# Performance work log

Hardware: AMD Instinct MI355X
Metric: run time of the kernel (lower is better)

Reference implementation:

```python
import jax, jax.numpy as jnp
import numpy as np

N_NODES = 100000
N_EDGES = 1000000
D = 64
HID = 64
OUT = 64
N_CLS = 10
N_GRAPHS = 512
BN_EPS = 1e-5


def setup_inputs() -> dict:
    key = jax.random.key(0)
    ks = jax.random.split(key, 16)
    inp = {
        "x": jax.random.normal(ks[0], (N_NODES, D), dtype=jnp.float32),
        "edge_index": jax.random.randint(ks[1], (2, N_EDGES), 0, N_NODES, dtype=jnp.int32),
        "batch": jnp.sort(jax.random.randint(ks[2], (N_NODES,), 0, N_GRAPHS, dtype=jnp.int32)),
    }
    def lin(k, fi, fo):
        lim = 1.0 / np.sqrt(fi)
        kw, kb = jax.random.split(k)
        return (jax.random.uniform(kw, (fi, fo), minval=-lim, maxval=lim, dtype=jnp.float32),
                jax.random.uniform(kb, (fo,), minval=-lim, maxval=lim, dtype=jnp.float32))
    # conv0 MLP([64,64,64]) with BN after first linear
    inp["w0a"], inp["b0a"] = lin(ks[3], D, HID)
    inp["g0"] = jnp.ones((HID,), jnp.float32); inp["be0"] = jnp.zeros((HID,), jnp.float32)
    inp["m0"] = jnp.zeros((HID,), jnp.float32); inp["v0"] = jnp.ones((HID,), jnp.float32)
    inp["w0b"], inp["b0b"] = lin(ks[4], HID, HID)
    # conv1 MLP([64,64,64])
    inp["w1a"], inp["b1a"] = lin(ks[5], HID, HID)
    inp["g1"] = jnp.ones((HID,), jnp.float32); inp["be1"] = jnp.zeros((HID,), jnp.float32)
    inp["m1"] = jnp.zeros((HID,), jnp.float32); inp["v1"] = jnp.ones((HID,), jnp.float32)
    inp["w1b"], inp["b1b"] = lin(ks[6], HID, OUT)
    # classifier
    inp["wc"], inp["bc"] = lin(ks[7], OUT, N_CLS)
    return inp


def _bn_eval(h, g, b, m, v):
    return (h - m) * jax.lax.rsqrt(v + BN_EPS) * g + b


def _mlp(h, wa, ba, g, be, m, v, wb, bb):
    # Linear -> BN -> ReLU -> (dropout eval=identity) -> Linear
    h = h @ wa + ba
    h = jax.nn.relu(_bn_eval(h, g, be, m, v))
    return h @ wb + bb


def _gin_conv(h, src, dst, wa, ba, g, be, m, v, wb, bb):
    # GINConv eps=0: mlp(x + sum_{j->i} x_j), messages scatter-added at dst
    agg = jax.ops.segment_sum(h[src], dst, num_segments=N_NODES)
    return _mlp(h + agg, wa, ba, g, be, m, v, wb, bb)


def reference(x, edge_index, batch,
              w0a, b0a, g0, be0, m0, v0, w0b, b0b,
              w1a, b1a, g1, be1, m1, v1, w1b, b1b,
              wc, bc):
    src, dst = edge_index[0], edge_index[1]
    h = _gin_conv(x, src, dst, w0a, b0a, g0, be0, m0, v0, w0b, b0b)
    h = jax.nn.relu(h)  # dropout is identity in eval
    h = _gin_conv(h, src, dst, w1a, b1a, g1, be1, m1, v1, w1b, b1b)
    # global mean pool over batch indices
    sums = jax.ops.segment_sum(h, batch, num_segments=N_GRAPHS)
    cnts = jax.ops.segment_sum(jnp.ones((h.shape[0],), h.dtype), batch, num_segments=N_GRAPHS)
    pooled = sums / jnp.maximum(cnts, 1.0)[:, None]
    return pooled @ wc + bc
```

## Files before the change

kernel.cpp:

```cpp
#include <hip/hip_runtime.h>

#define N_NODES 100000
#define N_EDGES 1000000
#define N_GRAPHS 512
#define N_CLS 10
#define BN_EPS 1e-5f

#define SCAN_NB 200
#define NTILES2 3125

typedef _Float16 half8 __attribute__((ext_vector_type(8)));
typedef _Float16 half4v __attribute__((ext_vector_type(4)));
typedef float floatx4 __attribute__((ext_vector_type(4)));

__global__ __launch_bounds__(256) void prep_kernel(
    const float* __restrict__ x, _Float16* __restrict__ xh,
    const int* __restrict__ batch, const int* __restrict__ dstI,
    int* __restrict__ deg, int* __restrict__ rank,
    const float* __restrict__ w0a, const float* __restrict__ b0a,
    const float* __restrict__ g0, const float* __restrict__ be0,
    const float* __restrict__ m0, const float* __restrict__ v0,
    const float* __restrict__ w0b,
    const float* __restrict__ w1a, const float* __restrict__ b1a,
    const float* __restrict__ g1, const float* __restrict__ be1,
    const float* __restrict__ m1, const float* __restrict__ v1,
    const float* __restrict__ w1b,
    int* __restrict__ gstart,
    _Float16* __restrict__ wHi, _Float16* __restrict__ wLo,
    float* __restrict__ b1p0, float* __restrict__ b1p1) {
    const int gid = blockIdx.x * 256 + threadIdx.x;

    if (gid < 1600000) {
        float4 v = ((const float4*)x)[gid];
        half4v h = {(_Float16)v.x, (_Float16)v.y, (_Float16)v.z, (_Float16)v.w};
        ((half4v*)xh)[gid] = h;
    }

    if (gid < N_EDGES)
        rank[gid] = atomicAdd(&deg[dstI[gid]], 1);

    if (gid <= N_NODES) {
        int bcur = (gid < N_NODES) ? batch[gid] : N_GRAPHS;
        int bprev = (gid > 0) ? batch[gid - 1] : -1;
        for (int g = bprev + 1; g <= bcur; ++g) gstart[g] = gid;
    }

    if (gid < 16384) {
        const int e = gid & 4095, mat = gid >> 12;
        const int jj = e & 7, lane = (e >> 3) & 63, c = (e >> 9) & 3, k0 = (e >> 11) & 1;
        const int k = k0 * 32 + (lane >> 4) * 8 + jj;
        const int col = c * 16 + (lane & 15);
        float val;
        if (mat == 0)      val = w0a[k * 64 + col] * (rsqrtf(v0[col] + BN_EPS) * g0[col]);
        else if (mat == 1) val = w0b[k * 64 + col];
        else if (mat == 2) val = w1a[k * 64 + col] * (rsqrtf(v1[col] + BN_EPS) * g1[col]);
        else               val = w1b[k * 64 + col];
        _Float16 hi = (_Float16)val;
        wHi[gid] = hi;
        wLo[gid] = (_Float16)(val - (float)hi);
    }

    if (gid >= 16384 && gid < 16512) {
        int t = gid - 16384;
        if (t < 64) {
            float s = rsqrtf(v0[t] + BN_EPS) * g0[t];
            b1p0[t] = (b0a[t] - m0[t]) * s + be0[t];
        } else {
            t -= 64;
            float s = rsqrtf(v1[t] + BN_EPS) * g1[t];
            b1p1[t] = (b1a[t] - m1[t]) * s + be1[t];
        }
    }
}

__global__ __launch_bounds__(256) void scanA_kernel(const int* __restrict__ deg,
                                                    int* __restrict__ bsum) {
    __shared__ int sh[256];
    const int base = blockIdx.x * 512;
    const int t = threadIdx.x;
    int a = 0, b = 0;
    if (base + t < N_NODES) a = deg[base + t];
    if (base + 256 + t < N_NODES) b = deg[base + 256 + t];
    sh[t] = a + b;
    __syncthreads();
#pragma unroll
    for (int off = 128; off > 0; off >>= 1) {
        if (t < off) sh[t] += sh[t + off];
        __syncthreads();
    }
    if (t == 0) bsum[blockIdx.x] = sh[0];
}

__global__ __launch_bounds__(256) void scanC_kernel(const int* __restrict__ deg,
                                                    const int* __restrict__ bsum,
                                                    int* __restrict__ rowptr) {
    __shared__ int sh[256];
    __shared__ int sboff[256];
    const int base = blockIdx.x * 512;
    const int t = threadIdx.x;

    const int bv = (t < SCAN_NB) ? bsum[t] : 0;
    sboff[t] = bv;

    const int i0 = base + 2 * t, i1 = i0 + 1;
    const int d0 = (i0 < N_NODES) ? deg[i0] : 0;
    const int d1 = (i1 < N_NODES) ? deg[i1] : 0;
    const int p = d0 + d1;
    sh[t] = p;
    __syncthreads();
#pragma unroll
    for (int off = 1; off < 256; off <<= 1) {
        int u = (t >= off) ? sh[t - off] : 0;
        int ub = (t >= off) ? sboff[t - off] : 0;
        __syncthreads();
        sh[t] += u;
        sboff[t] += ub;
        __syncthreads();
    }
    const int myoff = (blockIdx.x == 0) ? 0 : sboff[blockIdx.x - 1];
    const int excl = myoff + sh[t] - p;
    if (i0 < N_NODES) rowptr[i0] = excl;
    if (i1 < N_NODES) rowptr[i1] = excl + d0;
    if (blockIdx.x == 0 && t == 0) rowptr[N_NODES] = N_EDGES;
}

__global__ __launch_bounds__(256) void fill_kernel(const int* __restrict__ srcI,
                                                   const int* __restrict__ dstI,
                                                   const int* __restrict__ rank,
                                                   const int* __restrict__ rowptr,
                                                   int* __restrict__ sortedSrc) {
    int e = blockIdx.x * 256 + threadIdx.x;
    if (e >= N_EDGES) return;
    sortedSrc[rowptr[dstI[e]] + rank[e]] = srcI[e];
}

__device__ __forceinline__ int swz(int row, int col) {
    return row * 64 + (col ^ ((row & 7) << 3));
}

__device__ __forceinline__ void idx_stage(const int* __restrict__ srcList, int rpv,
                                          int mq, int nodeSel, int slotSel, int& idxOwn) {
    const int rr0 = __shfl(rpv, mq * 4 + nodeSel, 64);
    const int rr1 = __shfl(rpv, mq * 4 + nodeSel + 1, 64);
    const int c = rr1 - rr0;
    const int e0 = (c > 0) ? min(slotSel, c - 1) : 0;
    int pos = rr0 + e0;
    pos = min(pos, N_EDGES - 1);
    idxOwn = srcList[pos];
}

__device__ __forceinline__ void rows_stage(const _Float16* __restrict__ in, int rpv,
                                           int mq, int strip0, int eoff, int lf,
                                           int idxOwn, half4v (&vT)[4][4], half4v (&sS)[4]) {
    const int m0 = mq * 4;
#pragma unroll
    for (int i = 0; i < 4; ++i) {
        sS[i] = (half4v){0, 0, 0, 0};
        if (eoff == 0)
            sS[i] = *(const half4v*)(in + (size_t)(strip0 + m0 + i) * 64 + lf * 4);
    }
#pragma unroll
    for (int i = 0; i < 4; ++i) {
        const int rr0 = __builtin_amdgcn_readlane(rpv, m0 + i);
        const int rr1 = __builtin_amdgcn_readlane(rpv, m0 + i + 1);
        const int cI = rr1 - rr0;
        const int g = (min(cI, 16) + 3) >> 2;
#pragma unroll
        for (int k = 0; k < 4; ++k) {
            vT[i][k] = (half4v){0, 0, 0, 0};
            if (k < g) {
                const int id = __shfl(idxOwn, i * 16 + 4 * k + eoff, 64);
                vT[i][k] = *(const half4v*)(in + (size_t)id * 64 + lf * 4);
            }
        }
    }
}

__device__ __forceinline__ void consume_stage(const _Float16* __restrict__ in,
                                              const int* __restrict__ srcList, int rpv,
                                              int mq, int eoff, int lf, int j,
                                              const half4v (&vT)[4][4], const half4v (&sS)[4],
                                              _Float16* aggH, _Float16* aggL) {
    const int m0 = mq * 4;
#pragma unroll
    for (int i = 0; i < 4; ++i) {
        const int rr0 = __builtin_amdgcn_readlane(rpv, m0 + i);
        const int rr1 = __builtin_amdgcn_readlane(rpv, m0 + i + 1);
        const int cI = rr1 - rr0;
        float aR[4] = {0.f, 0.f, 0.f, 0.f};
#pragma unroll
        for (int k = 0; k < 4; ++k) {
            if (4 * k + eoff < cI) {
                aR[0] += (float)vT[i][k].x; aR[1] += (float)vT[i][k].y;
                aR[2] += (float)vT[i][k].z; aR[3] += (float)vT[i][k].w;
            }
        }
        for (int eb = 16; eb < cI; eb += 16) {
#pragma unroll
            for (int k = 0; k < 4; ++k) {
                const int e_ = eb + 4 * k + eoff;
                if (e_ < cI) {
                    const int id = srcList[rr0 + e_];
                    half4v t = *(const half4v*)(in + (size_t)id * 64 + lf * 4);
                    aR[0] += (float)t.x; aR[1] += (float)t.y;
                    aR[2] += (float)t.z; aR[3] += (float)t.w;
                }
            }
        }
        if (eoff == 0) {
            aR[0] += (float)sS[i].x; aR[1] += (float)sS[i].y;
            aR[2] += (float)sS[i].z; aR[3] += (float)sS[i].w;
        }
#pragma unroll
        for (int q = 0; q < 4; ++q) {
            aR[q] += __shfl_xor(aR[q], 16, 64);
            aR[q] += __shfl_xor(aR[q], 32, 64);
        }
        if (j < 16) {
            half4v hi, lo;
#pragma unroll
            for (int q = 0; q < 4; ++q) {
                hi[q] = (_Float16)aR[q];
                lo[q] = (_Float16)(aR[q] - (float)hi[q]);
            }
            const int idx = swz(m0 + i, 4 * j);
            *(half4v*)(aggH + idx) = hi;
            *(half4v*)(aggL + idx) = lo;
        }
    }
}

#define SBAR() __builtin_amdgcn_sched_barrier(0)

template <int POOL>
__global__ __launch_bounds__(128, 4) void conv_mfma(
    const _Float16* __restrict__ in, const int* __restrict__ rowptr,
    const int* __restrict__ srcList,
    const _Float16* __restrict__ wH1, const _Float16* __restrict__ wL1,
    const _Float16* __restrict__ wH2, const _Float16* __restrict__ wL2,
    const float* __restrict__ b1, const float* __restrict__ b2,
    _Float16* __restrict__ out, const int* __restrict__ batch,
    float* __restrict__ pooled) {
    __shared__ __align__(16) unsigned char scratch[2][4096];

    const int tid = threadIdx.x;
    const int j = tid & 63, wv = tid >> 6;
    const int eoff = j >> 4;
    const int lf = j & 15;
    const int base = blockIdx.x * 32;
    const int strip0 = base + wv * 16;

    int bb = 0;
    if (POOL) bb = batch[strip0 + min(j, 15)];

    const int rpv = rowptr[strip0 + min(j, 16)];

    _Float16* aggH = (_Float16*)scratch[wv];
    _Float16* aggL = aggH + 1024;

    {
        int idxA, idxB, idxC;
        half4v vA[4][4], vB[4][4], sA[4], sB[4];

        idx_stage(srcList, rpv, 0, eoff, lf, idxA);
        idx_stage(srcList, rpv, 1, eoff, lf, idxB);
        SBAR();
        rows_stage(in, rpv, 0, strip0, eoff, lf, idxA, vA, sA);
        SBAR();
        idx_stage(srcList, rpv, 2, eoff, lf, idxC);
        SBAR();
        rows_stage(in, rpv, 1, strip0, eoff, lf, idxB, vB, sB);
        SBAR();
        consume_stage(in, srcList, rpv, 0, eoff, lf, j, vA, sA, aggH, aggL);
        SBAR();
        idx_stage(srcList, rpv, 3, eoff, lf, idxA);
        SBAR();
        rows_stage(in, rpv, 2, strip0, eoff, lf, idxC, vA, sA);
        SBAR();
        consume_stage(in, srcList, rpv, 1, eoff, lf, j, vB, sB, aggH, aggL);
        SBAR();
        rows_stage(in, rpv, 3, strip0, eoff, lf, idxA, vB, sB);
        SBAR();
        consume_stage(in, srcList, rpv, 2, eoff, lf, j, vA, sA, aggH, aggL);
        SBAR();
        consume_stage(in, srcList, rpv, 3, eoff, lf, j, vB, sB, aggH, aggL);
    }

    const int l15 = j & 15, quad = j >> 4;
    const floatx4 vzero = {0.f, 0.f, 0.f, 0.f};

    floatx4 acc[4] = {vzero, vzero, vzero, vzero};
    {
#pragma unroll
        for (int k0 = 0; k0 < 2; ++k0) {
            const int aidx = swz(l15, quad * 8 + k0 * 32);
            half8 aH = *(const half8*)(aggH + aidx);
            half8 aL = *(const half8*)(aggL + aidx);
#pragma unroll
            for (int c = 0; c < 4; ++c) {
                const int fo = ((k0 * 4 + c) * 64 + j) * 8;
                half8 bH = *(const half8*)(wH1 + fo);
                half8 bL = *(const half8*)(wL1 + fo);
                acc[c] = __builtin_amdgcn_mfma_f32_16x16x32_f16(aH, bH, acc[c], 0, 0, 0);
                acc[c] = __builtin_amdgcn_mfma_f32_16x16x32_f16(aL, bH, acc[c], 0, 0, 0);
                acc[c] = __builtin_amdgcn_mfma_f32_16x16x32_f16(aH, bL, acc[c], 0, 0, 0);
            }
        }
    }
    _Float16* hH = aggH;
    _Float16* hL = aggL;
#pragma unroll
    for (int c = 0; c < 4; ++c) {
        const float bv = b1[c * 16 + l15];
#pragma unroll
        for (int r = 0; r < 4; ++r) {
            const int idx = swz(quad * 4 + r, c * 16 + l15);
            float v = acc[c][r] + bv;
            v = fmaxf(v, 0.f);
            const _Float16 hi = (_Float16)v;
            hH[idx] = hi;
            hL[idx] = (_Float16)(v - (float)hi);
        }
    }

    floatx4 acc2[4] = {vzero, vzero, vzero, vzero};
    {
#pragma unroll
        for (int k0 = 0; k0 < 2; ++k0) {
            const int aidx = swz(l15, quad * 8 + k0 * 32);
            half8 aH = *(const half8*)(hH + aidx);
            half8 aL = *(const half8*)(hL + aidx);
#pragma unroll
            for (int c = 0; c < 4; ++c) {
                const int fo = ((k0 * 4 + c) * 64 + j) * 8;
                half8 bH = *(const half8*)(wH2 + fo);
                half8 bL = *(const half8*)(wL2 + fo);
                acc2[c] = __builtin_amdgcn_mfma_f32_16x16x32_f16(aH, bH, acc2[c], 0, 0, 0);
                acc2[c] = __builtin_amdgcn_mfma_f32_16x16x32_f16(aL, bH, acc2[c], 0, 0, 0);
                acc2[c] = __builtin_amdgcn_mfma_f32_16x16x32_f16(aH, bL, acc2[c], 0, 0, 0);
            }
        }
    }

    if (!POOL) {
#pragma unroll
        for (int c = 0; c < 4; ++c) {
            const float bv = b2[c * 16 + l15];
#pragma unroll
            for (int r = 0; r < 4; ++r) {
                const int node = strip0 + quad * 4 + r;
                out[(size_t)node * 64 + c * 16 + l15] =
                    (_Float16)fmaxf(acc2[c][r] + bv, 0.f);
            }
        }
    } else {
        float* oT = (float*)scratch[wv];
#pragma unroll
        for (int c = 0; c < 4; ++c) {
            const float bv = b2[c * 16 + l15];
#pragma unroll
            for (int r = 0; r < 4; ++r)
                oT[(quad * 4 + r) * 64 + c * 16 + l15] = acc2[c][r] + bv;
        }
        __builtin_amdgcn_s_waitcnt(0);
        int curB = -1;
        float accv = 0.f;
#pragma unroll
        for (int r = 0; r < 16; ++r) {
            const int b = __builtin_amdgcn_readlane(bb, r);
            const float v = oT[r * 64 + j];
            if (b != curB) {
                if (curB >= 0) atomicAdd(&pooled[curB * 64 + j], accv);
                curB = b;
                accv = v;
            } else {
                accv += v;
            }
        }
        atomicAdd(&pooled[curB * 64 + j], accv);
    }
}

__global__ __launch_bounds__(64) void classifier_kernel(const float* __restrict__ pooled,
                                                        const int* __restrict__ gstart,
                                                        const float* __restrict__ wc,
                                                        const float* __restrict__ bc,
                                                        float* __restrict__ out) {
    const int g = blockIdx.x;
    const int j = threadIdx.x;
    const float c = fmaxf((float)(gstart[g + 1] - gstart[g]), 1.f);
    const float mean = pooled[g * 64 + j] / c;
#pragma unroll
    for (int cc = 0; cc < N_CLS; ++cc) {
        float p = mean * wc[j * N_CLS + cc];
#pragma unroll
        for (int off = 32; off > 0; off >>= 1) p += __shfl_down(p, off, 64);
        if (j == 0) out[g * N_CLS + cc] = p + bc[cc];
    }
}


extern "C" void kernel_launch(void* const* d_in, const int* in_sizes, int n_in,
                              void* d_out, int out_size, void* d_ws, size_t ws_size,
                              hipStream_t stream) {
    const float* x   = (const float*)d_in[0];
    const int*   ei  = (const int*)d_in[1];
    const int* batch = (const int*)d_in[2];
    const float* w0a = (const float*)d_in[3];
    const float* b0a = (const float*)d_in[4];
    const float* g0  = (const float*)d_in[5];
    const float* be0 = (const float*)d_in[6];
    const float* m0  = (const float*)d_in[7];
    const float* v0  = (const float*)d_in[8];
    const float* w0b = (const float*)d_in[9];
    const float* b0b = (const float*)d_in[10];
    const float* w1a = (const float*)d_in[11];
    const float* b1a = (const float*)d_in[12];
    const float* g1  = (const float*)d_in[13];
    const float* be1 = (const float*)d_in[14];
    const float* m1  = (const float*)d_in[15];
    const float* v1  = (const float*)d_in[16];
    const float* w1b = (const float*)d_in[17];
    const float* b1b = (const float*)d_in[18];
    const float* wc  = (const float*)d_in[19];
    const float* bc  = (const float*)d_in[20];
    float* out = (float*)d_out;

    const int* srcI = ei;
    const int* dstI = ei + N_EDGES;

    int* ws = (int*)d_ws;
    int*      deg       = ws;
    int*      bsum      = ws + 100000;
    float*    pooled    = (float*)(ws + 100404);
    int*      rowptr    = ws + 133172;
    int*      rank      = ws + 233176;
    int*      sortedSrc = ws + 1233176;
    _Float16* xh        = (_Float16*)(ws + 2233176);
    _Float16* h1        = (_Float16*)(ws + 5433176);
    float*    b1p0      = (float*)(ws + 8633176);
    float*    b1p1      = (float*)(ws + 8633240);
    int*      gstart    = ws + 8633304;
    _Float16* wHi       = (_Float16*)(ws + 8633820);
    _Float16* wLo       = (_Float16*)(ws + 8642012);

    (void)hipMemsetAsync((void*)deg, 0, 133172 * sizeof(int), stream);
    prep_kernel<<<6250, 256, 0, stream>>>(x, xh, batch, dstI, deg, rank,
                                          w0a, b0a, g0, be0, m0, v0, w0b,
                                          w1a, b1a, g1, be1, m1, v1, w1b,
                                          gstart, wHi, wLo, b1p0, b1p1);

    scanA_kernel<<<SCAN_NB, 256, 0, stream>>>(deg, bsum);
    scanC_kernel<<<SCAN_NB, 256, 0, stream>>>(deg, bsum, rowptr);
    fill_kernel<<<(N_EDGES + 255) / 256, 256, 0, stream>>>(srcI, dstI, rank, rowptr, sortedSrc);

    conv_mfma<0><<<NTILES2, 128, 0, stream>>>(xh, rowptr, sortedSrc,
                                              wHi, wLo, wHi + 4096, wLo + 4096,
                                              b1p0, b0b, h1, nullptr, nullptr);

    conv_mfma<1><<<NTILES2, 128, 0, stream>>>(h1, rowptr, sortedSrc,
                                              wHi + 8192, wLo + 8192, wHi + 12288, wLo + 12288,
                                              b1p1, b1b, nullptr, batch, pooled);

    classifier_kernel<<<N_GRAPHS, 64, 0, stream>>>(pooled, gstart, wc, bc, out);
}
```

Baseline: 279.1 us.

## Merge memset, prep, scan and fill stages into one cooperative kernel

Replaces the memset, the prep kernel, the two scan kernels and the CSR fill kernel with a single cooperative launch of 1024 blocks. Grid-wide syncs separate the phases: zeroing and conversion, the degree atomics, the block sums, the prefix scan and the fill. Work is spread with grid-stride loops. The goal is to remove several launch and inter-kernel gaps, but each grid.sync has its own cost and the fixed grid size may reduce parallelism in the atomic and fill phases.

```diff
diff --git a/kernel.cpp b/kernel.cpp
--- a/kernel.cpp
+++ b/kernel.cpp
@@ -1,4 +1,7 @@
 #include <hip/hip_runtime.h>
+#include <hip/hip_cooperative_groups.h>
+
+namespace cg = cooperative_groups;
 
 #define N_NODES 100000
 #define N_EDGES 1000000
@@ -8,15 +11,20 @@
 
 #define SCAN_NB 200
 #define NTILES2 3125
+#define COOP_NB 1024
 
 typedef _Float16 half8 __attribute__((ext_vector_type(8)));
 typedef _Float16 half4v __attribute__((ext_vector_type(4)));
 typedef float floatx4 __attribute__((ext_vector_type(4)));
 
-__global__ __launch_bounds__(256) void prep_kernel(
+__global__ __launch_bounds__(256) void prologue_kernel(
     const float* __restrict__ x, _Float16* __restrict__ xh,
-    const int* __restrict__ batch, const int* __restrict__ dstI,
+    const int* __restrict__ batch,
+    const int* __restrict__ srcI, const int* __restrict__ dstI,
     int* __restrict__ deg, int* __restrict__ rank,
+    int* __restrict__ bsum, int* __restrict__ rowptr,
+    int* __restrict__ sortedSrc,
+    int* __restrict__ gstart,
     const float* __restrict__ w0a, const float* __restrict__ b0a,
     const float* __restrict__ g0, const float* __restrict__ be0,
     const float* __restrict__ m0, const float* __restrict__ v0,
@@ -25,28 +33,31 @@
     const float* __restrict__ g1, const float* __restrict__ be1,
     const float* __restrict__ m1, const float* __restrict__ v1,
     const float* __restrict__ w1b,
-    int* __restrict__ gstart,
     _Float16* __restrict__ wHi, _Float16* __restrict__ wLo,
     float* __restrict__ b1p0, float* __restrict__ b1p1) {
-    const int gid = blockIdx.x * 256 + threadIdx.x;
-
-    if (gid < 1600000) {
-        float4 v = ((const float4*)x)[gid];
+    __shared__ int sh[256];
+    __shared__ int sboff[256];
+
+    cg::grid_group grid = cg::this_grid();
+    const int tid0 = blockIdx.x * 256 + threadIdx.x;
+    const int NTH = COOP_NB * 256;
+
+    for (int i = tid0; i < 133172; i += NTH) deg[i] = 0;
+
+    for (int i = tid0; i < 1600000; i += NTH) {
+        float4 v = ((const float4*)x)[i];
         half4v h = {(_Float16)v.x, (_Float16)v.y, (_Float16)v.z, (_Float16)v.w};
-        ((half4v*)xh)[gid] = h;
-    }
-
-    if (gid < N_EDGES)
-        rank[gid] = atomicAdd(&deg[dstI[gid]], 1);
-
-    if (gid <= N_NODES) {
-        int bcur = (gid < N_NODES) ? batch[gid] : N_GRAPHS;
-        int bprev = (gid > 0) ? batch[gid - 1] : -1;
-        for (int g = bprev + 1; g <= bcur; ++g) gstart[g] = gid;
-    }
-
-    if (gid < 16384) {
-        const int e = gid & 4095, mat = gid >> 12;
+        ((half4v*)xh)[i] = h;
+    }
+
+    for (int i = tid0; i <= N_NODES; i += NTH) {
+        int bcur = (i < N_NODES) ? batch[i] : N_GRAPHS;
+        int bprev = (i > 0) ? batch[i - 1] : -1;
+        for (int g = bprev + 1; g <= bcur; ++g) gstart[g] = i;
+    }
+
+    if (tid0 < 16384) {
+        const int e = tid0 & 4095, mat = tid0 >> 12;
         const int jj = e & 7, lane = (e >> 3) & 63, c = (e >> 9) & 3, k0 = (e >> 11) & 1;
         const int k = k0 * 32 + (lane >> 4) * 8 + jj;
         const int col = c * 16 + (lane & 15);
@@ -56,12 +67,10 @@
         else if (mat == 2) val = w1a[k * 64 + col] * (rsqrtf(v1[col] + BN_EPS) * g1[col]);
         else               val = w1b[k * 64 + col];
         _Float16 hi = (_Float16)val;
-        wHi[gid] = hi;
-        wLo[gid] = (_Float16)(val - (float)hi);
-    }
-
-    if (gid >= 16384 && gid < 16512) {
-        int t = gid - 16384;
+        wHi[tid0] = hi;
+        wLo[tid0] = (_Float16)(val - (float)hi);
+    } else if (tid0 < 16512) {
+        int t = tid0 - 16384;
         if (t < 64) {
             float s = rsqrtf(v0[t] + BN_EPS) * g0[t];
             b1p0[t] = (b0a[t] - m0[t]) * s + be0[t];
@@ -71,67 +80,65 @@
             b1p1[t] = (b1a[t] - m1[t]) * s + be1[t];
         }
     }
-}
-
-__global__ __launch_bounds__(256) void scanA_kernel(const int* __restrict__ deg,
-                                                    int* __restrict__ bsum) {
-    __shared__ int sh[256];
-    const int base = blockIdx.x * 512;
-    const int t = threadIdx.x;
-    int a = 0, b = 0;
-    if (base + t < N_NODES) a = deg[base + t];
-    if (base + 256 + t < N_NODES) b = deg[base + 256 + t];
-    sh[t] = a + b;
-    __syncthreads();
-#pragma unroll
-    for (int off = 128; off > 0; off >>= 1) {
-        if (t < off) sh[t] += sh[t + off];
+
+    grid.sync();
+
+    for (int e = tid0; e < N_EDGES; e += NTH)
+        rank[e] = atomicAdd(&deg[dstI[e]], 1);
+
+    grid.sync();
+
+    if (blockIdx.x < SCAN_NB) {
+        const int base = blockIdx.x * 512;
+        const int t = threadIdx.x;
+        int a = 0, b = 0;
+        if (base + t < N_NODES) a = deg[base + t];
+        if (base + 256 + t < N_NODES) b = deg[base + 256 + t];
+        sh[t] = a + b;
         __syncthreads();
-    }
-    if (t == 0) bsum[blockIdx.x] = sh[0];
-}
-
-__global__ __launch_bounds__(256) void scanC_kernel(const int* __restrict__ deg,
-                                                    const int* __restrict__ bsum,
-                                                    int* __restrict__ rowptr) {
-    __shared__ int sh[256];
-    __shared__ int sboff[256];
-    const int base = blockIdx.x * 512;
-    const int t = threadIdx.x;
-
-    const int bv = (t < SCAN_NB) ? bsum[t] : 0;
-    sboff[t] = bv;
-
-    const int i0 = base + 2 * t, i1 = i0 + 1;
-    const int d0 = (i0 < N_NODES) ? deg[i0] : 0;
-    const int d1 = (i1 < N_NODES) ? deg[i1] : 0;
-    const int p = d0 + d1;
-    sh[t] = p;
-    __syncthreads();
-#pragma unroll
-    for (int off = 1; off < 256; off <<= 1) {
-        int u = (t >= off) ? sh[t - off] : 0;
-        int ub = (t >= off) ? sboff[t - off] : 0;
+#pragma unroll
+        for (int off = 128; off > 0; off >>= 1) {
+            if (t < off) sh[t] += sh[t + off];
+            __syncthreads();
+        }
+        if (t == 0) bsum[blockIdx.x] = sh[0];
+    }
+
+    grid.sync();
+
+    if (blockIdx.x < SCAN_NB) {
+        const int base = blockIdx.x * 512;
+        const int t = threadIdx.x;
+
+        const int bv = (t < SCAN_NB) ? bsum[t] : 0;
+        sboff[t] = bv;
+
+        const int i0 = base + 2 * t, i1 = i0 + 1;
+        const int d0 = (i0 < N_NODES) ? deg[i0] : 0;
+        const int d1 = (i1 < N_NODES) ? deg[i1] : 0;
+        const int p = d0 + d1;
+        sh[t] = p;
         __syncthreads();
-        sh[t] += u;
-        sboff[t] += ub;
-        __syncthreads();
-    }
-    const int myoff = (blockIdx.x == 0) ? 0 : sboff[blockIdx.x - 1];
-    const int excl = myoff + sh[t] - p;
-    if (i0 < N_NODES) rowptr[i0] = excl;
-    if (i1 < N_NODES) rowptr[i1] = excl + d0;
-    if (blockIdx.x == 0 && t == 0) rowptr[N_NODES] = N_EDGES;
-}
-
-__global__ __launch_bounds__(256) void fill_kernel(const int* __restrict__ srcI,
-                                                   const int* __restrict__ dstI,
-                                                   const int* __restrict__ rank,
-                                                   const int* __restrict__ rowptr,
-                                                   int* __restrict__ sortedSrc) {
-    int e = blockIdx.x * 256 + threadIdx.x;
-    if (e >= N_EDGES) return;
-    sortedSrc[rowptr[dstI[e]] + rank[e]] = srcI[e];
+#pragma unroll
+        for (int off = 1; off < 256; off <<= 1) {
+            int u = (t >= off) ? sh[t - off] : 0;
+            int ub = (t >= off) ? sboff[t - off] : 0;
+            __syncthreads();
+            sh[t] += u;
+            sboff[t] += ub;
+            __syncthreads();
+        }
+        const int myoff = (blockIdx.x == 0) ? 0 : sboff[blockIdx.x - 1];
+        const int excl = myoff + sh[t] - p;
+        if (i0 < N_NODES) rowptr[i0] = excl;
+        if (i1 < N_NODES) rowptr[i1] = excl + d0;
+        if (blockIdx.x == 0 && t == 0) rowptr[N_NODES] = N_EDGES;
+    }
+
+    grid.sync();
+
+    for (int e = tid0; e < N_EDGES; e += NTH)
+        sortedSrc[rowptr[dstI[e]] + rank[e]] = srcI[e];
 }
 
 __device__ __forceinline__ int swz(int row, int col) {
@@ -444,15 +451,33 @@
     _Float16* wHi       = (_Float16*)(ws + 8633820);
     _Float16* wLo       = (_Float16*)(ws + 8642012);
 
-    (void)hipMemsetAsync((void*)deg, 0, 133172 * sizeof(int), stream);
-    prep_kernel<<<6250, 256, 0, stream>>>(x, xh, batch, dstI, deg, rank,
-                                          w0a, b0a, g0, be0, m0, v0, w0b,
-                                          w1a, b1a, g1, be1, m1, v1, w1b,
-                                          gstart, wHi, wLo, b1p0, b1p1);
-
-    scanA_kernel<<<SCAN_NB, 256, 0, stream>>>(deg, bsum);
-    scanC_kernel<<<SCAN_NB, 256, 0, stream>>>(deg, bsum, rowptr);
-    fill_kernel<<<(N_EDGES + 255) / 256, 256, 0, stream>>>(srcI, dstI, rank, rowptr, sortedSrc);
+    {
+        const float* xA = x; _Float16* xhA = xh; const int* batchA = batch;
+        const int* srcA = srcI; const int* dstA = dstI;
+        int* degA = deg; int* rankA = rank; int* bsumA = bsum; int* rowptrA = rowptr;
+        int* sortedA = sortedSrc; int* gstartA = gstart;
+        const float* w0aA = w0a; const float* b0aA = b0a;
+        const float* g0A = g0; const float* be0A = be0;
+        const float* m0A = m0; const float* v0A = v0;
+        const float* w0bA = w0b;
+        const float* w1aA = w1a; const float* b1aA = b1a;
+        const float* g1A = g1; const float* be1A = be1;
+        const float* m1A = m1; const float* v1A = v1;
+        const float* w1bA = w1b;
+        _Float16* wHiA = wHi; _Float16* wLoA = wLo;
+        float* b1p0A = b1p0; float* b1p1A = b1p1;
+        void* cargs[] = {
+            (void*)&xA, (void*)&xhA, (void*)&batchA, (void*)&srcA, (void*)&dstA,
+            (void*)&degA, (void*)&rankA, (void*)&bsumA, (void*)&rowptrA,
+            (void*)&sortedA, (void*)&gstartA,
+            (void*)&w0aA, (void*)&b0aA, (void*)&g0A, (void*)&be0A,
+            (void*)&m0A, (void*)&v0A, (void*)&w0bA,
+            (void*)&w1aA, (void*)&b1aA, (void*)&g1A, (void*)&be1A,
+            (void*)&m1A, (void*)&v1A, (void*)&w1bA,
+            (void*)&wHiA, (void*)&wLoA, (void*)&b1p0A, (void*)&b1p1A};
+        (void)hipLaunchCooperativeKernel(reinterpret_cast<void*>(prologue_kernel),
+                                         dim3(COOP_NB), dim3(256), cargs, 0, stream);
+    }
 
     conv_mfma<0><<<NTILES2, 128, 0, stream>>>(xh, rowptr, sortedSrc,
                                               wHi, wLo, wHi + 4096, wLo + 4096,
```

After: 715.5 us. 156% more time.

## Fold degree scan into prep kernel via last-block ticket

Applied to the files above, without the earlier changes.

Removes the two separate scan kernels and instead has the last block of the prep kernel, chosen by an atomic ticket counter, compute the exclusive prefix sum of node degrees to build rowptr. The aim is to save two kernel launches and their inter-kernel gaps. The cost is that a single 256-thread block now serially scans 100k entries, with each thread walking 391 strided elements, so the access pattern is uncoalesced and all of this runs on one CU at the tail of prep. The ticket lives in the memset region, so it is reset on every call.

```diff
diff --git a/kernel.cpp b/kernel.cpp
--- a/kernel.cpp
+++ b/kernel.cpp
@@ -6,8 +6,8 @@
 #define N_CLS 10
 #define BN_EPS 1e-5f
 
-#define SCAN_NB 200
 #define NTILES2 3125
+#define PREP_NB 6250
 
 typedef _Float16 half8 __attribute__((ext_vector_type(8)));
 typedef _Float16 half4v __attribute__((ext_vector_type(4)));
@@ -17,6 +17,7 @@
     const float* __restrict__ x, _Float16* __restrict__ xh,
     const int* __restrict__ batch, const int* __restrict__ dstI,
     int* __restrict__ deg, int* __restrict__ rank,
+    int* __restrict__ rowptr, int* __restrict__ ticket,
     const float* __restrict__ w0a, const float* __restrict__ b0a,
     const float* __restrict__ g0, const float* __restrict__ be0,
     const float* __restrict__ m0, const float* __restrict__ v0,
@@ -28,6 +29,9 @@
     int* __restrict__ gstart,
     _Float16* __restrict__ wHi, _Float16* __restrict__ wLo,
     float* __restrict__ b1p0, float* __restrict__ b1p1) {
+    __shared__ int sh[256];
+    __shared__ int lastBlk;
+
     const int gid = blockIdx.x * 256 + threadIdx.x;
 
     if (gid < 1600000) {
@@ -71,57 +75,43 @@
             b1p1[t] = (b1a[t] - m1[t]) * s + be1[t];
         }
     }
-}
-
-__global__ __launch_bounds__(256) void scanA_kernel(const int* __restrict__ deg,
-                                                    int* __restrict__ bsum) {
-    __shared__ int sh[256];
-    const int base = blockIdx.x * 512;
+
+    __threadfence();
+    __syncthreads();
+    if (threadIdx.x == 0)
+        lastBlk = (atomicAdd(ticket, 1) == PREP_NB - 1) ? 1 : 0;
+    __syncthreads();
+    if (!lastBlk) return;
+
     const int t = threadIdx.x;
-    int a = 0, b = 0;
-    if (base + t < N_NODES) a = deg[base + t];
-    if (base + 256 + t < N_NODES) b = deg[base + 256 + t];
-    sh[t] = a + b;
-    __syncthreads();
-#pragma unroll
-    for (int off = 128; off > 0; off >>= 1) {
-        if (t < off) sh[t] += sh[t + off];
-        __syncthreads();
-    }
-    if (t == 0) bsum[blockIdx.x] = sh[0];
-}
-
-__global__ __launch_bounds__(256) void scanC_kernel(const int* __restrict__ deg,
-                                                    const int* __restrict__ bsum,
-                                                    int* __restrict__ rowptr) {
-    __shared__ int sh[256];
-    __shared__ int sboff[256];
-    const int base = blockIdx.x * 512;
-    const int t = threadIdx.x;
-
-    const int bv = (t < SCAN_NB) ? bsum[t] : 0;
-    sboff[t] = bv;
-
-    const int i0 = base + 2 * t, i1 = i0 + 1;
-    const int d0 = (i0 < N_NODES) ? deg[i0] : 0;
-    const int d1 = (i1 < N_NODES) ? deg[i1] : 0;
-    const int p = d0 + d1;
-    sh[t] = p;
+    const int C = 391;
+    const int i0 = t * C;
+    int s = 0;
+#pragma unroll 8
+    for (int k = 0; k < C; ++k) {
+        const int i = i0 + k;
+        if (i < N_NODES)
+            s += __hip_atomic_load(&deg[i], __ATOMIC_RELAXED, __HIP_MEMORY_SCOPE_AGENT);
+    }
+    sh[t] = s;
     __syncthreads();
 #pragma unroll
     for (int off = 1; off < 256; off <<= 1) {
         int u = (t >= off) ? sh[t - off] : 0;
-        int ub = (t >= off) ? sboff[t - off] : 0;
         __syncthreads();
         sh[t] += u;
-        sboff[t] += ub;
         __syncthreads();
     }
-    const int myoff = (blockIdx.x == 0) ? 0 : sboff[blockIdx.x - 1];
-    const int excl = myoff + sh[t] - p;
-    if (i0 < N_NODES) rowptr[i0] = excl;
-    if (i1 < N_NODES) rowptr[i1] = excl + d0;
-    if (blockIdx.x == 0 && t == 0) rowptr[N_NODES] = N_EDGES;
+    int run = (t > 0) ? sh[t - 1] : 0;
+#pragma unroll 8
+    for (int k = 0; k < C; ++k) {
+        const int i = i0 + k;
+        if (i < N_NODES) {
+            rowptr[i] = run;
+            run += __hip_atomic_load(&deg[i], __ATOMIC_RELAXED, __HIP_MEMORY_SCOPE_AGENT);
+        }
+    }
+    if (t == 255) rowptr[N_NODES] = N_EDGES;
 }
 
 __global__ __launch_bounds__(256) void fill_kernel(const int* __restrict__ srcI,
@@ -431,7 +421,7 @@
 
     int* ws = (int*)d_ws;
     int*      deg       = ws;
-    int*      bsum      = ws + 100000;
+    int*      ticket    = ws + 100300;
     float*    pooled    = (float*)(ws + 100404);
     int*      rowptr    = ws + 133172;
     int*      rank      = ws + 233176;
@@ -445,13 +435,13 @@
     _Float16* wLo       = (_Float16*)(ws + 8642012);
 
     (void)hipMemsetAsync((void*)deg, 0, 133172 * sizeof(int), stream);
-    prep_kernel<<<6250, 256, 0, stream>>>(x, xh, batch, dstI, deg, rank,
-                                          w0a, b0a, g0, be0, m0, v0, w0b,
-                                          w1a, b1a, g1, be1, m1, v1, w1b,
-                                          gstart, wHi, wLo, b1p0, b1p1);
-
-    scanA_kernel<<<SCAN_NB, 256, 0, stream>>>(deg, bsum);
-    scanC_kernel<<<SCAN_NB, 256, 0, stream>>>(deg, bsum, rowptr);
+
+    prep_kernel<<<PREP_NB, 256, 0, stream>>>(x, xh, batch, dstI, deg, rank,
+                                             rowptr, ticket,
+                                             w0a, b0a, g0, be0, m0, v0, w0b,
+                                             w1a, b1a, g1, be1, m1, v1, w1b,
+                                             gstart, wHi, wLo, b1p0, b1p1);
+
     fill_kernel<<<(N_EDGES + 255) / 256, 256, 0, stream>>>(srcI, dstI, rank, rowptr, sortedSrc);
 
     conv_mfma<0><<<NTILES2, 128, 0, stream>>>(xh, rowptr, sortedSrc,
```

Result: slower. 940.3 us (+236.9%).
